# Performance work log

Measured on AMD Instinct MI355X. Metric: run time of the kernel, lower is better.

The kernel has to match this reference:

```python
import jax, jax.numpy as jnp
import numpy as np

B, C, D, H, W = 2, 3, 128, 160, 160
RANGE_FLOW = 0.4


def setup_inputs() -> dict:
    key = jax.random.key(0)
    k1, k2 = jax.random.split(key)
    flow_1 = jax.random.normal(k1, (B, C, D, H, W), dtype=jnp.float32)
    flow_2 = jax.random.normal(k2, (B, C, D, H, W), dtype=jnp.float32)
    # identity sampling grid in voxel coords, channel order (x, y, z)
    zz, yy, xx = jnp.meshgrid(
        jnp.arange(D, dtype=jnp.float32),
        jnp.arange(H, dtype=jnp.float32),
        jnp.arange(W, dtype=jnp.float32),
        indexing='ij')
    sample_grid = jnp.broadcast_to(jnp.stack([xx, yy, zz], axis=-1), (B, D, H, W, 3))
    range_flow = jnp.float32(RANGE_FLOW)
    return {"flow_1": flow_1, "flow_2": flow_2, "sample_grid": sample_grid,
            "range_flow": range_flow}


def grid_sample_3d_border(vol, grid):
    """PyTorch F.grid_sample 3D, mode='bilinear' (trilinear), align_corners=True,
    padding_mode='border'. vol: [B,C,D,H,W], grid: [B,D,H,W,3] normalized (x,y,z)."""
    Bv, Cv, Dv, Hv, Wv = vol.shape
    # unnormalize (align_corners=True) and clamp to border
    x = jnp.clip((grid[..., 0] + 1.0) * 0.5 * (Wv - 1), 0.0, Wv - 1)
    y = jnp.clip((grid[..., 1] + 1.0) * 0.5 * (Hv - 1), 0.0, Hv - 1)
    z = jnp.clip((grid[..., 2] + 1.0) * 0.5 * (Dv - 1), 0.0, Dv - 1)
    x0f, y0f, z0f = jnp.floor(x), jnp.floor(y), jnp.floor(z)
    wx, wy, wz = x - x0f, y - y0f, z - z0f  # fractional weights [B,D,H,W]
    ix0 = x0f.astype(jnp.int32); ix1 = jnp.minimum(ix0 + 1, Wv - 1)
    iy0 = y0f.astype(jnp.int32); iy1 = jnp.minimum(iy0 + 1, Hv - 1)
    iz0 = z0f.astype(jnp.int32); iz1 = jnp.minimum(iz0 + 1, Dv - 1)

    vol_flat = vol.reshape(Bv, Cv, -1)  # [B,C,D*H*W]
    gD, gH, gW = grid.shape[1:4]

    def gather(iz, iy, ix):
        idx = ((iz * Hv + iy) * Wv + ix).reshape(Bv, 1, -1)
        return jnp.take_along_axis(vol_flat, idx, axis=2).reshape(Bv, Cv, gD, gH, gW)

    # broadcast weights over channel dim
    wx = wx[:, None]; wy = wy[:, None]; wz = wz[:, None]
    c000 = gather(iz0, iy0, ix0); c001 = gather(iz0, iy0, ix1)
    c010 = gather(iz0, iy1, ix0); c011 = gather(iz0, iy1, ix1)
    c100 = gather(iz1, iy0, ix0); c101 = gather(iz1, iy0, ix1)
    c110 = gather(iz1, iy1, ix0); c111 = gather(iz1, iy1, ix1)
    c00 = c000 * (1 - wx) + c001 * wx
    c01 = c010 * (1 - wx) + c011 * wx
    c10 = c100 * (1 - wx) + c101 * wx
    c11 = c110 * (1 - wx) + c111 * wx
    c0 = c00 * (1 - wy) + c01 * wy
    c1 = c10 * (1 - wy) + c11 * wy
    return c0 * (1 - wz) + c1 * wz


def reference(flow_1, flow_2, sample_grid, range_flow):
    Dv, Hv, Wv = sample_grid.shape[1:4]
    g = sample_grid + jnp.transpose(flow_1, (0, 2, 3, 4, 1)) * range_flow
    # normalize each coordinate channel to [-1, 1] (align_corners convention)
    gx = 2.0 * g[..., 0] / (Wv - 1) - 1.0
    gy = 2.0 * g[..., 1] / (Hv - 1) - 1.0
    gz = 2.0 * g[..., 2] / (Dv - 1) - 1.0
    grid = jnp.stack([gx, gy, gz], axis=-1)
    return grid_sample_3d_border(flow_2, grid) + flow_1
```

## Files before the change

kernel.cpp:

```cpp
#include <hip/hip_runtime.h>


constexpr int DD = 128, HH = 160, WW = 160;
constexpr int HW = HH * WW;
constexpr int SP = DD * HW;
constexpr int TX = 32, TH = 8, TD = 8;
constexpr int PX = 40, PY = 12, PZ = 12;
constexpr int PHF = PX * PY * PZ;
constexpr int VSLOT = PHF / 4;
constexpr int VPAD = VSLOT + 32;
constexpr int NTX = WW / TX, NTH = HH / TH, NTD = DD / TD;
constexpr int NB = 2 * NTX * NTH * NTD;

#define AS1 __attribute__((address_space(1)))
#define AS3 __attribute__((address_space(3)))

__global__ __launch_bounds__(256, 4) void comp_xform_db(
    const float* __restrict__ f1,
    const float* __restrict__ f2,
    const float* __restrict__ rfp,
    float* __restrict__ out)
{
    __shared__ __align__(16) float4 slab[2][VPAD];

    const int tid = threadIdx.x;

    const int bid = blockIdx.x;
    const int wg  = (bid & 7) * (NB / 8) + (bid >> 3);

    const int tx = wg % NTX; int r_ = wg / NTX;
    const int th = r_ % NTH; r_ /= NTH;
    const int td = r_ % NTD; const int b = r_ / NTD;

    const int x0 = tx * TX, h0 = th * TH, d0 = td * TD;
    const int xlo = x0 - 4, ylo = h0 - 2, zlo = d0 - 2;

    const size_t boff = (size_t)b * (size_t)(3 * SP);
    const float* __restrict__ f1b = f1 + boff;
    const float* __restrict__ f2b = f2 + boff;
    float* __restrict__ ob = out + boff;

    const float rf = rfp[0];

    const int wl = tid & 31, hh = tid >> 5;
    const int w = x0 + wl, h = h0 + hh;
    const int sp0 = (d0 * HH + h) * WW + w;
    const int wbase = tid & 192;

    int goff[6];
#pragma unroll
    for (int r = 0; r < 6; ++r) {
        const int s = r * 256 + tid;
        const int row = s / 10, k = s - row * 10;
        const int rz = row / PY, ry = row - rz * PY;
        const int gz = min(max(zlo + rz, 0), DD - 1);
        const int gy = min(max(ylo + ry, 0), HH - 1);
        const int gx = min(max(xlo + 4 * k, 0), WW - 4);
        goff[r] = (s < VSLOT) ? ((gz * HH + gy) * WW + gx) : -1;
    }

    auto stage = [&](int buf, const float* __restrict__ src) {
#pragma unroll
        for (int r = 0; r < 6; ++r) {
            if (goff[r] >= 0) {
                const float* gp = src + goff[r];
                AS3 void* lp = (AS3 void*)&slab[buf][r * 256 + wbase];
                __builtin_amdgcn_global_load_lds((const AS1 void*)gp, lp, 16, 0, 0);
            }
        }
    };

    stage(0, f2b);

    float f1s0[8], f1s1[8], f1s2[8];
#pragma unroll
    for (int dd = 0; dd < TD; ++dd) {
        const int sp = sp0 + dd * HW;
        f1s0[dd] = f1b[sp];
        f1s1[dd] = f1b[SP + sp];
        f1s2[dd] = f1b[2 * SP + sp];
    }

    int voff[8]; float wxs[8], wys[8], wzs[8]; unsigned okm = 0;
#pragma unroll
    for (int dd = 0; dd < TD; ++dd) {
        const float x = fminf(fmaxf((float)w + rf * f1s0[dd], 0.f), (float)(WW - 1));
        const float y = fminf(fmaxf((float)h + rf * f1s1[dd], 0.f), (float)(HH - 1));
        const float z = fminf(fmaxf((float)(d0 + dd) + rf * f1s2[dd], 0.f), (float)(DD - 1));
        const float fx = floorf(x), fy = floorf(y), fz = floorf(z);
        const int rx = (int)fx - xlo, ry = (int)fy - ylo, rz = (int)fz - zlo;
        const bool ok = ((unsigned)rx <= 38u) & ((unsigned)ry <= 10u) & ((unsigned)rz <= 10u);
        okm |= (ok ? 1u : 0u) << dd;
        voff[dd] = ok ? ((rz * PY + ry) * PX + rx) : 0;
        wxs[dd] = ok ? (x - fx) : x;
        wys[dd] = ok ? (y - fy) : y;
        wzs[dd] = ok ? (z - fz) : z;
    }

    __syncthreads();

#pragma unroll
    for (int c = 0; c < 3; ++c) {
        if (c < 2) stage((c + 1) & 1, f2b + (size_t)(c + 1) * SP);

        const float* __restrict__ br  = (const float*)slab[c & 1];
        const float* __restrict__ f2c = f2b + (size_t)c * SP;
        float* __restrict__ oc = ob + (size_t)c * SP;

#pragma unroll
        for (int dd = 0; dd < TD; ++dd) {
            const float* p = br + voff[dd];
            const float wx = wxs[dd], wy = wys[dd], wz = wzs[dd];
            const float ax = 1.f - wx, ay = 1.f - wy, az = 1.f - wz;
            const float a0 = p[0],            a1 = p[1];
            const float b0 = p[PX],           b1 = p[PX + 1];
            const float c0 = p[PX * PY],      c1 = p[PX * PY + 1];
            const float e0 = p[PX * PY + PX], e1 = p[PX * PY + PX + 1];
            const float top = ay * fmaf(a0, ax, a1 * wx) + wy * fmaf(b0, ax, b1 * wx);
            const float bot = ay * fmaf(c0, ax, c1 * wx) + wy * fmaf(e0, ax, e1 * wx);
            const float res = az * top + wz * bot;
            const float f1c = (c == 0) ? f1s0[dd] : ((c == 1) ? f1s1[dd] : f1s2[dd]);
            oc[sp0 + dd * HW] = res + f1c;
        }

        if (okm != 255u) {
#pragma unroll
            for (int dd = 0; dd < TD; ++dd) {
                if (!((okm >> dd) & 1u)) {
                    const float X = wxs[dd], Y = wys[dd], Z = wzs[dd];
                    const float fx = floorf(X), fy = floorf(Y), fz = floorf(Z);
                    const float wx = X - fx, wy = Y - fy, wz = Z - fz;
                    const int ix0 = (int)fx, iy0 = (int)fy, iz0 = (int)fz;
                    const int ix1 = min(ix0 + 1, WW - 1);
                    const int iy1 = min(iy0 + 1, HH - 1);
                    const int iz1 = min(iz0 + 1, DD - 1);
                    const int q00 = (iz0 * HH + iy0) * WW, q01 = (iz0 * HH + iy1) * WW;
                    const int q10 = (iz1 * HH + iy0) * WW, q11 = (iz1 * HH + iy1) * WW;
                    const float c000 = f2c[q00 + ix0], c001 = f2c[q00 + ix1];
                    const float c010 = f2c[q01 + ix0], c011 = f2c[q01 + ix1];
                    const float c100 = f2c[q10 + ix0], c101 = f2c[q10 + ix1];
                    const float c110 = f2c[q11 + ix0], c111 = f2c[q11 + ix1];
                    const float ax = 1.f - wx, ay = 1.f - wy, az = 1.f - wz;
                    const float top = ay * (c000 * ax + c001 * wx) + wy * (c010 * ax + c011 * wx);
                    const float bot = ay * (c100 * ax + c101 * wx) + wy * (c110 * ax + c111 * wx);
                    const float f1c = (c == 0) ? f1s0[dd] : ((c == 1) ? f1s1[dd] : f1s2[dd]);
                    oc[sp0 + dd * HW] = az * top + wz * bot + f1c;
                }
            }
        }

        if (c < 2) __syncthreads();
    }
}

extern "C" void kernel_launch(void* const* d_in, const int* in_sizes, int n_in,
                              void* d_out, int out_size, void* d_ws, size_t ws_size,
                              hipStream_t stream) {
    const float* f1  = (const float*)d_in[0];
    const float* f2  = (const float*)d_in[1];
    const float* rfp = (const float*)d_in[3];
    float* out = (float*)d_out;

    comp_xform_db<<<NB, 256, 0, stream>>>(f1, f2, rfp, out);
}
```

Measured before the change: 49.30 us.

## Replace double-buffered LDS slab with single 64-wide padded slab

Widens the staged halo row from 40 to 64 floats so index math uses shifts and the per-run bounds check disappears. Drops double buffering: one LDS slab is refilled between channels behind two barriers. This removes the guarded loads and lowers LDS footprint, which may help occupancy, but it loads more redundant halo data and no longer overlaps the next channel's load with the current channel's compute.

```diff
diff --git a/kernel.cpp b/kernel.cpp
--- a/kernel.cpp
+++ b/kernel.cpp
@@ -5,23 +5,23 @@
 constexpr int HW = HH * WW;
 constexpr int SP = DD * HW;
 constexpr int TX = 32, TH = 8, TD = 8;
-constexpr int PX = 40, PY = 12, PZ = 12;
+constexpr int PX = 64, PY = 12, PZ = 12;
 constexpr int PHF = PX * PY * PZ;
 constexpr int VSLOT = PHF / 4;
-constexpr int VPAD = VSLOT + 32;
+constexpr int RUNS = VSLOT / 256;
 constexpr int NTX = WW / TX, NTH = HH / TH, NTD = DD / TD;
 constexpr int NB = 2 * NTX * NTH * NTD;
 
 #define AS1 __attribute__((address_space(1)))
 #define AS3 __attribute__((address_space(3)))
 
-__global__ __launch_bounds__(256, 4) void comp_xform_db(
+__global__ __launch_bounds__(256, 4) void comp_xform_px64(
     const float* __restrict__ f1,
     const float* __restrict__ f2,
     const float* __restrict__ rfp,
     float* __restrict__ out)
 {
-    __shared__ __align__(16) float4 slab[2][VPAD];
+    __shared__ __align__(16) float slab[PHF];
 
     const int tid = threadIdx.x;
 
@@ -47,30 +47,28 @@
     const int sp0 = (d0 * HH + h) * WW + w;
     const int wbase = tid & 192;
 
-    int goff[6];
+    int goff[RUNS];
 #pragma unroll
-    for (int r = 0; r < 6; ++r) {
+    for (int r = 0; r < RUNS; ++r) {
         const int s = r * 256 + tid;
-        const int row = s / 10, k = s - row * 10;
+        const int row = s >> 4, k = s & 15;
         const int rz = row / PY, ry = row - rz * PY;
         const int gz = min(max(zlo + rz, 0), DD - 1);
         const int gy = min(max(ylo + ry, 0), HH - 1);
         const int gx = min(max(xlo + 4 * k, 0), WW - 4);
-        goff[r] = (s < VSLOT) ? ((gz * HH + gy) * WW + gx) : -1;
+        goff[r] = (gz * HH + gy) * WW + gx;
     }
 
-    auto stage = [&](int buf, const float* __restrict__ src) {
+    auto stage = [&](const float* __restrict__ src) {
 #pragma unroll
-        for (int r = 0; r < 6; ++r) {
-            if (goff[r] >= 0) {
-                const float* gp = src + goff[r];
-                AS3 void* lp = (AS3 void*)&slab[buf][r * 256 + wbase];
-                __builtin_amdgcn_global_load_lds((const AS1 void*)gp, lp, 16, 0, 0);
-            }
+        for (int r = 0; r < RUNS; ++r) {
+            const float* gp = src + goff[r];
+            AS3 void* lp = (AS3 void*)&slab[(r * 256 + wbase) * 4];
+            __builtin_amdgcn_global_load_lds((const AS1 void*)gp, lp, 16, 0, 0);
         }
     };
 
-    stage(0, f2b);
+    stage(f2b);
 
     float f1s0[8], f1s1[8], f1s2[8];
 #pragma unroll
@@ -101,9 +99,7 @@
 
 #pragma unroll
     for (int c = 0; c < 3; ++c) {
-        if (c < 2) stage((c + 1) & 1, f2b + (size_t)(c + 1) * SP);
-
-        const float* __restrict__ br  = (const float*)slab[c & 1];
+        const float* __restrict__ br  = slab;
         const float* __restrict__ f2c = f2b + (size_t)c * SP;
         float* __restrict__ oc = ob + (size_t)c * SP;
 
@@ -149,7 +145,11 @@
             }
         }
 
-        if (c < 2) __syncthreads();
+        if (c < 2) {
+            __syncthreads();
+            stage(f2b + (size_t)(c + 1) * SP);
+            __syncthreads();
+        }
     }
 }
 
@@ -161,5 +161,5 @@
     const float* rfp = (const float*)d_in[3];
     float* out = (float*)d_out;
 
-    comp_xform_db<<<NB, 256, 0, stream>>>(f1, f2, rfp, out);
+    comp_xform_px64<<<NB, 256, 0, stream>>>(f1, f2, rfp, out);
 }
```

Result: faster. 45.62 us (-7.5%).
